# Optimization experiments

Measured on AMD Instinct MI355X. Metric: run time of the kernel, lower is better.

The kernel has to match this reference:

```python
import jax, jax.numpy as jnp
import numpy as np

BN_EPS = 1e-5

def setup_inputs() -> dict:
    key = jax.random.key(0)
    ks = jax.random.split(key, 8)
    B, C, H, W = 32, 256, 64, 64
    Cm, Co = 128, 256  # mid = max(8, 256//2), out = 256
    x = jax.random.normal(ks[0], (B, C, H, W), dtype=jnp.float32)
    w1 = jax.random.normal(ks[1], (Cm, C), dtype=jnp.float32) * 0.05
    b1 = jnp.zeros((Cm,), dtype=jnp.float32)
    bn_gamma = jnp.ones((Cm,), dtype=jnp.float32)
    bn_beta = jnp.zeros((Cm,), dtype=jnp.float32)
    bn_mean = jnp.zeros((Cm,), dtype=jnp.float32)
    bn_var = jnp.ones((Cm,), dtype=jnp.float32)
    w2 = jax.random.normal(ks[2], (Co, Cm), dtype=jnp.float32) * 0.05
    b2 = jnp.zeros((Co,), dtype=jnp.float32)
    w3 = jax.random.normal(ks[3], (Co, Cm), dtype=jnp.float32) * 0.05
    b3 = jnp.zeros((Co,), dtype=jnp.float32)
    return {"x": x, "w1": w1, "b1": b1, "bn_gamma": bn_gamma, "bn_beta": bn_beta,
            "bn_mean": bn_mean, "bn_var": bn_var, "w2": w2, "b2": b2, "w3": w3, "b3": b3}

def _hswish(y):
    return y * jnp.clip(y + 3.0, 0.0, 6.0) / 6.0

def reference(x, w1, b1, bn_gamma, bn_beta, bn_mean, bn_var, w2, b2, w3, b3):
    B, C, H, W = x.shape
    # pool_h: mean over W -> [B,C,H]; pool_w: mean over H -> [B,C,W] (after permute)
    xh = jnp.mean(x, axis=3)  # [B,C,H]
    xw = jnp.mean(x, axis=2)  # [B,C,W]
    y = jnp.concatenate([xh, xw], axis=2)  # [B,C,H+W]
    # 1x1 conv as matmul over channel dim
    y = jnp.einsum('mc,bcl->bml', w1, y) + b1[None, :, None]  # [B,Cm,H+W]
    # BatchNorm (inference, running stats)
    y = (y - bn_mean[None, :, None]) * (bn_gamma[None, :, None] * jax.lax.rsqrt(bn_var + BN_EPS)[None, :, None]) + bn_beta[None, :, None]
    y = _hswish(y)
    ah, aw = y[:, :, :H], y[:, :, H:]  # [B,Cm,H], [B,Cm,W]
    gh = jax.nn.sigmoid(jnp.einsum('om,bmh->boh', w2, ah) + b2[None, :, None])  # [B,Co,H]
    gw = jax.nn.sigmoid(jnp.einsum('om,bmw->bow', w3, aw) + b3[None, :, None])  # [B,Co,W]
    return x * gh[:, :, :, None] * gw[:, :, None, :]
```

## Files before the change

### kernel.cpp

```cpp
#include <hip/hip_runtime.h>

#define NB 32
#define NC 256
#define NL 128
#define NCM 128
#define NCO 256
#define NPLANES (NB * NC)

__global__ __launch_bounds__(256) void k_pool(const float* __restrict__ x,
                                              float* __restrict__ pool) {
    int t = threadIdx.x;
    __shared__ float smem[1024];
    #pragma unroll
    for (int p = 0; p < 4; ++p) {
        int plane = blockIdx.x * 4 + p;
        const float4* px = (const float4*)(x + (size_t)plane * 4096);
        float4 csum = make_float4(0.f, 0.f, 0.f, 0.f);
        #pragma unroll
        for (int i = 0; i < 4; ++i) {
            int f = t + i * 256;
            float4 v = px[f];
            csum.x += v.x; csum.y += v.y; csum.z += v.z; csum.w += v.w;
            float s = v.x + v.y + v.z + v.w;
            s += __shfl_xor(s, 1);
            s += __shfl_xor(s, 2);
            s += __shfl_xor(s, 4);
            s += __shfl_xor(s, 8);
            if ((t & 15) == 0)
                pool[(size_t)plane * NL + (t >> 4) + 16 * i] = s * 0.015625f;
        }
        ((float4*)smem)[t] = csum;
        __syncthreads();
        if (t < 64) {
            float acc = 0.f;
            #pragma unroll
            for (int g = 0; g < 16; ++g)
                acc += smem[((t >> 2) + 16 * g) * 4 + (t & 3)];
            pool[(size_t)plane * NL + 64 + t] = acc * 0.015625f;
        }
        __syncthreads();
    }
}

__global__ __launch_bounds__(256) void k_mlp1(const float* __restrict__ pool,
                                              const float* __restrict__ w1,
                                              const float* __restrict__ b1,
                                              const float* __restrict__ gam,
                                              const float* __restrict__ bet,
                                              const float* __restrict__ mu,
                                              const float* __restrict__ var,
                                              float* __restrict__ a) {
    int b = blockIdx.x, m0 = blockIdx.y * 16;
    int t = threadIdx.x;
    __shared__ float w1t[32][16];
    __shared__ float pt[32][NL];
    const float* poolb = pool + (size_t)b * NC * NL;
    int tm = t & 7;
    int tl = t >> 3;
    float acc[2][4] = {};

    for (int cc = 0; cc < NC; cc += 32) {
        {
            int mi = t & 15, c0 = (t >> 4) * 2;
            float2 wv = *(const float2*)(w1 + (size_t)(m0 + mi) * NC + cc + c0);
            w1t[c0 + 0][mi] = wv.x; w1t[c0 + 1][mi] = wv.y;
        }
        #pragma unroll
        for (int i = 0; i < 4; ++i) {
            int f = t + i * 256;
            int ci = f >> 5, l4 = f & 31;
            *(float4*)&pt[ci][l4 * 4] =
                *(const float4*)(poolb + (size_t)(cc + ci) * NL + l4 * 4);
        }
        __syncthreads();
        #pragma unroll
        for (int cj = 0; cj < 32; ++cj) {
            float2 wv = *(const float2*)&w1t[cj][tm * 2];
            float4 pv = *(const float4*)&pt[cj][tl * 4];
            float pa[4] = {pv.x, pv.y, pv.z, pv.w};
            #pragma unroll
            for (int j = 0; j < 4; ++j) {
                acc[0][j] += wv.x * pa[j];
                acc[1][j] += wv.y * pa[j];
            }
        }
        __syncthreads();
    }
    #pragma unroll
    for (int i = 0; i < 2; ++i) {
        int m = m0 + tm * 2 + i;
        float scale = gam[m] * rsqrtf(var[m] + 1e-5f);
        float base = b1[m] - mu[m];
        float bb = bet[m];
        #pragma unroll
        for (int j = 0; j < 4; ++j) {
            float y = (acc[i][j] + base) * scale + bb;
            float hs = y * fminf(fmaxf(y + 3.f, 0.f), 6.f) * (1.f / 6.f);
            a[(size_t)b * NCM * NL + (size_t)m * NL + tl * 4 + j] = hs;
        }
    }
}

__global__ __launch_bounds__(256) void k_gate(const float* __restrict__ a,
                                              const float* __restrict__ w2,
                                              const float* __restrict__ b2,
                                              const float* __restrict__ w3,
                                              const float* __restrict__ b3,
                                              float* __restrict__ gh,
                                              float* __restrict__ gw) {
    int b = blockIdx.x, side = blockIdx.y, ot = blockIdx.z;
    const float* wsel = side ? w3 : w2;
    const float* bsel = side ? b3 : b2;
    float* gsel = side ? gw : gh;
    int t = threadIdx.x;
    __shared__ float wt[32][32];
    __shared__ float at[32][64];
    int to = t & 15;
    int th = t >> 4;
    float acc[2][4] = {};
    const float* ab = a + (size_t)b * NCM * NL + side * 64;

    for (int kc = 0; kc < NCM; kc += 32) {
        {
            int oi = t & 31, k0 = (t >> 5) * 4;
            float4 wv = *(const float4*)(wsel + (size_t)(ot * 32 + oi) * NCM + kc + k0);
            wt[k0 + 0][oi] = wv.x; wt[k0 + 1][oi] = wv.y;
            wt[k0 + 2][oi] = wv.z; wt[k0 + 3][oi] = wv.w;
        }
        #pragma unroll
        for (int i = 0; i < 2; ++i) {
            int f = t + i * 256;
            int ki = f >> 4, h4 = f & 15;
            *(float4*)&at[ki][h4 * 4] =
                *(const float4*)(ab + (size_t)(kc + ki) * NL + h4 * 4);
        }
        __syncthreads();
        #pragma unroll
        for (int kj = 0; kj < 32; ++kj) {
            float2 wv = *(const float2*)&wt[kj][to * 2];
            float4 av = *(const float4*)&at[kj][th * 4];
            float aa[4] = {av.x, av.y, av.z, av.w};
            #pragma unroll
            for (int j = 0; j < 4; ++j) {
                acc[0][j] += wv.x * aa[j];
                acc[1][j] += wv.y * aa[j];
            }
        }
        __syncthreads();
    }
    #pragma unroll
    for (int i = 0; i < 2; ++i) {
        int o = ot * 32 + to * 2 + i;
        float bias = bsel[o];
        #pragma unroll
        for (int j = 0; j < 4; ++j) {
            float v = acc[i][j] + bias;
            float g = 1.f / (1.f + __expf(-v));
            gsel[((size_t)b * NCO + o) * 64 + th * 4 + j] = g;
        }
    }
}

__global__ __launch_bounds__(256) void k_apply(const float* __restrict__ x,
                                               const float* __restrict__ gh,
                                               const float* __restrict__ gw,
                                               float* __restrict__ out) {
    int t = threadIdx.x;
    #pragma unroll
    for (int p = 0; p < 2; ++p) {
        int plane = blockIdx.x * 2 + p;
        const float4* px = (const float4*)(x + (size_t)plane * 4096);
        float4* po = (float4*)(out + (size_t)plane * 4096);
        const float* ghp = gh + (size_t)plane * 64;
        const float4* gwp = (const float4*)(gw + (size_t)plane * 64);
        #pragma unroll
        for (int i = 0; i < 4; ++i) {
            int f = t + i * 256;
            int row = f >> 4, w4 = f & 15;
            float4 v = px[f];
            float g = ghp[row];
            float4 gv = gwp[w4];
            v.x *= g * gv.x; v.y *= g * gv.y;
            v.z *= g * gv.z; v.w *= g * gv.w;
            po[f] = v;
        }
    }
}

extern "C" void kernel_launch(void* const* d_in, const int* in_sizes, int n_in,
                              void* d_out, int out_size, void* d_ws, size_t ws_size,
                              hipStream_t stream) {
    const float* x   = (const float*)d_in[0];
    const float* w1  = (const float*)d_in[1];
    const float* b1  = (const float*)d_in[2];
    const float* gam = (const float*)d_in[3];
    const float* bet = (const float*)d_in[4];
    const float* mu  = (const float*)d_in[5];
    const float* var = (const float*)d_in[6];
    const float* w2  = (const float*)d_in[7];
    const float* b2  = (const float*)d_in[8];
    const float* w3  = (const float*)d_in[9];
    const float* b3  = (const float*)d_in[10];
    float* ws   = (float*)d_ws;
    float* pool = ws;
    float* a    = ws + 1048576;
    float* gh   = ws + 1572864;
    float* gw   = ws + 2097152;
    float* out  = (float*)d_out;

    k_pool<<<NPLANES / 4, 256, 0, stream>>>(x, pool);
    k_mlp1<<<dim3(NB, 8), 256, 0, stream>>>(pool, w1, b1, gam, bet, mu, var, a);
    k_gate<<<dim3(NB, 2, 8), 256, 0, stream>>>(a, w2, b2, w3, b3, gh, gw);
    k_apply<<<NPLANES / 2, 256, 0, stream>>>(x, gh, gw, out);
}
```

Baseline: 85.87 us.

## Fuse pooling, MLP, gating and apply into one kernel with per-batch barriers

```diff
diff --git a/kernel.cpp b/kernel.cpp
--- a/kernel.cpp
+++ b/kernel.cpp
@@ -6,14 +6,49 @@
 #define NCM 128
 #define NCO 256
 #define NPLANES (NB * NC)
-
-__global__ __launch_bounds__(256) void k_pool(const float* __restrict__ x,
-                                              float* __restrict__ pool) {
-    int t = threadIdx.x;
-    __shared__ float smem[1024];
-    #pragma unroll
-    for (int p = 0; p < 4; ++p) {
-        int plane = blockIdx.x * 4 + p;
+#define SUBS 32
+
+typedef float v4f __attribute__((ext_vector_type(4)));
+
+__device__ __forceinline__ void st_coh(float* p, float v) {
+    __hip_atomic_store(p, v, __ATOMIC_RELAXED, __HIP_MEMORY_SCOPE_AGENT);
+}
+__device__ __forceinline__ float ld_coh(const float* p) {
+    return __hip_atomic_load(p, __ATOMIC_RELAXED, __HIP_MEMORY_SCOPE_AGENT);
+}
+
+__device__ __forceinline__ void batch_barrier(unsigned* cnt) {
+    __syncthreads();
+    if (threadIdx.x == 0) {
+        __hip_atomic_fetch_add(cnt, 1u, __ATOMIC_RELEASE,
+                               __HIP_MEMORY_SCOPE_AGENT);
+        while (__hip_atomic_load(cnt, __ATOMIC_RELAXED,
+                                 __HIP_MEMORY_SCOPE_AGENT) < (unsigned)SUBS)
+            __builtin_amdgcn_s_sleep(2);
+    }
+    __syncthreads();
+}
+
+__global__ __launch_bounds__(256, 4) void k_ca(
+    const float* __restrict__ x,
+    const float* __restrict__ w1, const float* __restrict__ b1,
+    const float* __restrict__ gam, const float* __restrict__ bet,
+    const float* __restrict__ mu, const float* __restrict__ var,
+    const float* __restrict__ w2, const float* __restrict__ b2,
+    const float* __restrict__ w3, const float* __restrict__ b3,
+    float* __restrict__ pool, float* __restrict__ a,
+    float* __restrict__ gh, float* __restrict__ gw,
+    unsigned* __restrict__ bar,
+    float* __restrict__ out)
+{
+    const int blk = blockIdx.x;
+    const int b   = blk >> 5;
+    const int sub = blk & 31;
+    const int t   = threadIdx.x;
+    __shared__ float smem[4608];
+
+    for (int p = 0; p < 8; ++p) {
+        int plane = b * NC + sub * 8 + p;
         const float4* px = (const float4*)(x + (size_t)plane * 4096);
         float4 csum = make_float4(0.f, 0.f, 0.f, 0.f);
         #pragma unroll
@@ -27,7 +62,8 @@
             s += __shfl_xor(s, 4);
             s += __shfl_xor(s, 8);
             if ((t & 15) == 0)
-                pool[(size_t)plane * NL + (t >> 4) + 16 * i] = s * 0.015625f;
+                st_coh(&pool[(size_t)plane * NL + (t >> 4) + 16 * i],
+                       s * 0.015625f);
         }
         ((float4*)smem)[t] = csum;
         __syncthreads();
@@ -36,153 +72,143 @@
             #pragma unroll
             for (int g = 0; g < 16; ++g)
                 acc += smem[((t >> 2) + 16 * g) * 4 + (t & 3)];
-            pool[(size_t)plane * NL + 64 + t] = acc * 0.015625f;
+            st_coh(&pool[(size_t)plane * NL + 64 + t], acc * 0.015625f);
         }
         __syncthreads();
     }
-}
-
-__global__ __launch_bounds__(256) void k_mlp1(const float* __restrict__ pool,
-                                              const float* __restrict__ w1,
-                                              const float* __restrict__ b1,
-                                              const float* __restrict__ gam,
-                                              const float* __restrict__ bet,
-                                              const float* __restrict__ mu,
-                                              const float* __restrict__ var,
-                                              float* __restrict__ a) {
-    int b = blockIdx.x, m0 = blockIdx.y * 16;
-    int t = threadIdx.x;
-    __shared__ float w1t[32][16];
-    __shared__ float pt[32][NL];
-    const float* poolb = pool + (size_t)b * NC * NL;
-    int tm = t & 7;
-    int tl = t >> 3;
-    float acc[2][4] = {};
-
-    for (int cc = 0; cc < NC; cc += 32) {
-        {
-            int mi = t & 15, c0 = (t >> 4) * 2;
-            float2 wv = *(const float2*)(w1 + (size_t)(m0 + mi) * NC + cc + c0);
-            w1t[c0 + 0][mi] = wv.x; w1t[c0 + 1][mi] = wv.y;
-        }
-        #pragma unroll
-        for (int i = 0; i < 4; ++i) {
-            int f = t + i * 256;
-            int ci = f >> 5, l4 = f & 31;
-            *(float4*)&pt[ci][l4 * 4] =
-                *(const float4*)(poolb + (size_t)(cc + ci) * NL + l4 * 4);
+    batch_barrier(&bar[b * 3 + 0]);
+
+    if (sub < 8) {
+        int m0 = sub * 16;
+        float* w1t = smem;
+        float* pt  = smem + 512;
+        const float* poolb = pool + (size_t)b * NC * NL;
+        int tm = t & 7, tl = t >> 3;
+        float acc[2][4] = {};
+        for (int cc = 0; cc < NC; cc += 32) {
+            {
+                int mi = t & 15, c0 = (t >> 4) * 2;
+                float2 wv = *(const float2*)(w1 + (size_t)(m0 + mi) * NC + cc + c0);
+                w1t[(c0 + 0) * 16 + mi] = wv.x;
+                w1t[(c0 + 1) * 16 + mi] = wv.y;
+            }
+            #pragma unroll
+            for (int k = 0; k < 16; ++k) {
+                int idx = t + k * 256;
+                int ci = idx >> 7, l = idx & 127;
+                pt[ci * 128 + l] = ld_coh(poolb + (size_t)(cc + ci) * NL + l);
+            }
+            __syncthreads();
+            #pragma unroll
+            for (int cj = 0; cj < 32; ++cj) {
+                float2 wv = *(const float2*)&w1t[cj * 16 + tm * 2];
+                float4 pv = *(const float4*)&pt[cj * 128 + tl * 4];
+                float pa[4] = {pv.x, pv.y, pv.z, pv.w};
+                #pragma unroll
+                for (int j = 0; j < 4; ++j) {
+                    acc[0][j] += wv.x * pa[j];
+                    acc[1][j] += wv.y * pa[j];
+                }
+            }
+            __syncthreads();
+        }
+        #pragma unroll
+        for (int i = 0; i < 2; ++i) {
+            int m = m0 + tm * 2 + i;
+            float scale = gam[m] * rsqrtf(var[m] + 1e-5f);
+            float base = b1[m] - mu[m];
+            float bb = bet[m];
+            #pragma unroll
+            for (int j = 0; j < 4; ++j) {
+                float y = (acc[i][j] + base) * scale + bb;
+                float hs = y * fminf(fmaxf(y + 3.f, 0.f), 6.f) * (1.f / 6.f);
+                st_coh(&a[(size_t)b * NCM * NL + (size_t)m * NL + tl * 4 + j], hs);
+            }
+        }
+    }
+    batch_barrier(&bar[b * 3 + 1]);
+
+    if (sub < 16) {
+        int side = sub >> 3, ot = sub & 7;
+        const float* wsel = side ? w3 : w2;
+        const float* bsel = side ? b3 : b2;
+        float* gsel = side ? gw : gh;
+        float* wt = smem;
+        float* at = smem + 1024;
+        int to = t & 15, th = t >> 4;
+        float acc[2][4] = {};
+        const float* ab = a + (size_t)b * NCM * NL + side * 64;
+        for (int kc = 0; kc < NCM; kc += 32) {
+            {
+                int oi = t & 31, k0 = (t >> 5) * 4;
+                float4 wv = *(const float4*)(wsel + (size_t)(ot * 32 + oi) * NCM + kc + k0);
+                wt[(k0 + 0) * 32 + oi] = wv.x; wt[(k0 + 1) * 32 + oi] = wv.y;
+                wt[(k0 + 2) * 32 + oi] = wv.z; wt[(k0 + 3) * 32 + oi] = wv.w;
+            }
+            #pragma unroll
+            for (int k = 0; k < 8; ++k) {
+                int idx = t + k * 256;
+                int ki = idx >> 6, h = idx & 63;
+                at[ki * 64 + h] = ld_coh(ab + (size_t)(kc + ki) * NL + h);
+            }
+            __syncthreads();
+            #pragma unroll
+            for (int kj = 0; kj < 32; ++kj) {
+                float2 wv = *(const float2*)&wt[kj * 32 + to * 2];
+                float4 av = *(const float4*)&at[kj * 64 + th * 4];
+                float aa[4] = {av.x, av.y, av.z, av.w};
+                #pragma unroll
+                for (int j = 0; j < 4; ++j) {
+                    acc[0][j] += wv.x * aa[j];
+                    acc[1][j] += wv.y * aa[j];
+                }
+            }
+            __syncthreads();
+        }
+        #pragma unroll
+        for (int i = 0; i < 2; ++i) {
+            int o = ot * 32 + to * 2 + i;
+            float bias = bsel[o];
+            #pragma unroll
+            for (int j = 0; j < 4; ++j) {
+                float v = acc[i][j] + bias;
+                float g = 1.f / (1.f + __expf(-v));
+                st_coh(&gsel[((size_t)b * NCO + o) * 64 + th * 4 + j], g);
+            }
+        }
+    }
+    batch_barrier(&bar[b * 3 + 2]);
+
+    {
+        float* gsm = smem;
+        int c0 = sub * 8;
+        #pragma unroll
+        for (int k = 0; k < 4; ++k) {
+            int idx = t + k * 256;
+            int p = idx >> 7, r = idx & 127;
+            size_t plane = (size_t)b * NC + c0 + p;
+            float v = (r < 64) ? ld_coh(&gh[plane * 64 + r])
+                               : ld_coh(&gw[plane * 64 + (r - 64)]);
+            gsm[p * 128 + r] = v;
         }
         __syncthreads();
-        #pragma unroll
-        for (int cj = 0; cj < 32; ++cj) {
-            float2 wv = *(const float2*)&w1t[cj][tm * 2];
-            float4 pv = *(const float4*)&pt[cj][tl * 4];
-            float pa[4] = {pv.x, pv.y, pv.z, pv.w};
-            #pragma unroll
-            for (int j = 0; j < 4; ++j) {
-                acc[0][j] += wv.x * pa[j];
-                acc[1][j] += wv.y * pa[j];
-            }
-        }
-        __syncthreads();
-    }
-    #pragma unroll
-    for (int i = 0; i < 2; ++i) {
-        int m = m0 + tm * 2 + i;
-        float scale = gam[m] * rsqrtf(var[m] + 1e-5f);
-        float base = b1[m] - mu[m];
-        float bb = bet[m];
-        #pragma unroll
-        for (int j = 0; j < 4; ++j) {
-            float y = (acc[i][j] + base) * scale + bb;
-            float hs = y * fminf(fmaxf(y + 3.f, 0.f), 6.f) * (1.f / 6.f);
-            a[(size_t)b * NCM * NL + (size_t)m * NL + tl * 4 + j] = hs;
-        }
-    }
-}
-
-__global__ __launch_bounds__(256) void k_gate(const float* __restrict__ a,
-                                              const float* __restrict__ w2,
-                                              const float* __restrict__ b2,
-                                              const float* __restrict__ w3,
-                                              const float* __restrict__ b3,
-                                              float* __restrict__ gh,
-                                              float* __restrict__ gw) {
-    int b = blockIdx.x, side = blockIdx.y, ot = blockIdx.z;
-    const float* wsel = side ? w3 : w2;
-    const float* bsel = side ? b3 : b2;
-    float* gsel = side ? gw : gh;
-    int t = threadIdx.x;
-    __shared__ float wt[32][32];
-    __shared__ float at[32][64];
-    int to = t & 15;
-    int th = t >> 4;
-    float acc[2][4] = {};
-    const float* ab = a + (size_t)b * NCM * NL + side * 64;
-
-    for (int kc = 0; kc < NCM; kc += 32) {
-        {
-            int oi = t & 31, k0 = (t >> 5) * 4;
-            float4 wv = *(const float4*)(wsel + (size_t)(ot * 32 + oi) * NCM + kc + k0);
-            wt[k0 + 0][oi] = wv.x; wt[k0 + 1][oi] = wv.y;
-            wt[k0 + 2][oi] = wv.z; wt[k0 + 3][oi] = wv.w;
-        }
-        #pragma unroll
-        for (int i = 0; i < 2; ++i) {
-            int f = t + i * 256;
-            int ki = f >> 4, h4 = f & 15;
-            *(float4*)&at[ki][h4 * 4] =
-                *(const float4*)(ab + (size_t)(kc + ki) * NL + h4 * 4);
-        }
-        __syncthreads();
-        #pragma unroll
-        for (int kj = 0; kj < 32; ++kj) {
-            float2 wv = *(const float2*)&wt[kj][to * 2];
-            float4 av = *(const float4*)&at[kj][th * 4];
-            float aa[4] = {av.x, av.y, av.z, av.w};
-            #pragma unroll
-            for (int j = 0; j < 4; ++j) {
-                acc[0][j] += wv.x * aa[j];
-                acc[1][j] += wv.y * aa[j];
-            }
-        }
-        __syncthreads();
-    }
-    #pragma unroll
-    for (int i = 0; i < 2; ++i) {
-        int o = ot * 32 + to * 2 + i;
-        float bias = bsel[o];
-        #pragma unroll
-        for (int j = 0; j < 4; ++j) {
-            float v = acc[i][j] + bias;
-            float g = 1.f / (1.f + __expf(-v));
-            gsel[((size_t)b * NCO + o) * 64 + th * 4 + j] = g;
-        }
-    }
-}
-
-__global__ __launch_bounds__(256) void k_apply(const float* __restrict__ x,
-                                               const float* __restrict__ gh,
-                                               const float* __restrict__ gw,
-                                               float* __restrict__ out) {
-    int t = threadIdx.x;
-    #pragma unroll
-    for (int p = 0; p < 2; ++p) {
-        int plane = blockIdx.x * 2 + p;
-        const float4* px = (const float4*)(x + (size_t)plane * 4096);
-        float4* po = (float4*)(out + (size_t)plane * 4096);
-        const float* ghp = gh + (size_t)plane * 64;
-        const float4* gwp = (const float4*)(gw + (size_t)plane * 64);
-        #pragma unroll
-        for (int i = 0; i < 4; ++i) {
-            int f = t + i * 256;
-            int row = f >> 4, w4 = f & 15;
-            float4 v = px[f];
-            float g = ghp[row];
-            float4 gv = gwp[w4];
-            v.x *= g * gv.x; v.y *= g * gv.y;
-            v.z *= g * gv.z; v.w *= g * gv.w;
-            po[f] = v;
+        for (int p = 0; p < 8; ++p) {
+            size_t plane = (size_t)b * NC + c0 + p;
+            const float4* px = (const float4*)(x + plane * 4096);
+            float4* po = (float4*)(out + plane * 4096);
+            const float* ghp = &gsm[p * 128];
+            const float4* gwp = (const float4*)&gsm[p * 128 + 64];
+            #pragma unroll
+            for (int i = 0; i < 4; ++i) {
+                int f = t + i * 256;
+                int row = f >> 4, w4 = f & 15;
+                float4 v = px[f];
+                float g = ghp[row];
+                float4 gv = gwp[w4];
+                v.x *= g * gv.x; v.y *= g * gv.y;
+                v.z *= g * gv.z; v.w *= g * gv.w;
+                po[f] = v;
+            }
         }
     }
 }
@@ -206,10 +232,11 @@
     float* a    = ws + 1048576;
     float* gh   = ws + 1572864;
     float* gw   = ws + 2097152;
+    unsigned* bar = (unsigned*)(ws + 2621440);
     float* out  = (float*)d_out;
 
-    k_pool<<<NPLANES / 4, 256, 0, stream>>>(x, pool);
-    k_mlp1<<<dim3(NB, 8), 256, 0, stream>>>(pool, w1, b1, gam, bet, mu, var, a);
-    k_gate<<<dim3(NB, 2, 8), 256, 0, stream>>>(a, w2, b2, w3, b3, gh, gw);
-    k_apply<<<NPLANES / 2, 256, 0, stream>>>(x, gh, gw, out);
-}
+    hipMemsetAsync(bar, 0, NB * 3 * sizeof(unsigned), stream);
+    k_ca<<<NB * SUBS, 256, 0, stream>>>(x, w1, b1, gam, bet, mu, var,
+                                        w2, b2, w3, b3,
+                                        pool, a, gh, gw, bar, out);
+}
```

After: 287.3 us. 235% more time.

## Fuse channel MLP and gate kernels, per-wave pooling without block sync

Applied to the files above, without the earlier changes.

```diff
diff --git a/kernel.cpp b/kernel.cpp
--- a/kernel.cpp
+++ b/kernel.cpp
@@ -7,157 +7,150 @@
 #define NCO 256
 #define NPLANES (NB * NC)
 
+typedef float v4f __attribute__((ext_vector_type(4)));
+
 __global__ __launch_bounds__(256) void k_pool(const float* __restrict__ x,
                                               float* __restrict__ pool) {
-    int t = threadIdx.x;
-    __shared__ float smem[1024];
-    #pragma unroll
-    for (int p = 0; p < 4; ++p) {
-        int plane = blockIdx.x * 4 + p;
-        const float4* px = (const float4*)(x + (size_t)plane * 4096);
-        float4 csum = make_float4(0.f, 0.f, 0.f, 0.f);
-        #pragma unroll
-        for (int i = 0; i < 4; ++i) {
-            int f = t + i * 256;
-            float4 v = px[f];
-            csum.x += v.x; csum.y += v.y; csum.z += v.z; csum.w += v.w;
-            float s = v.x + v.y + v.z + v.w;
-            s += __shfl_xor(s, 1);
-            s += __shfl_xor(s, 2);
-            s += __shfl_xor(s, 4);
-            s += __shfl_xor(s, 8);
-            if ((t & 15) == 0)
-                pool[(size_t)plane * NL + (t >> 4) + 16 * i] = s * 0.015625f;
-        }
-        ((float4*)smem)[t] = csum;
-        __syncthreads();
-        if (t < 64) {
-            float acc = 0.f;
-            #pragma unroll
-            for (int g = 0; g < 16; ++g)
-                acc += smem[((t >> 2) + 16 * g) * 4 + (t & 3)];
-            pool[(size_t)plane * NL + 64 + t] = acc * 0.015625f;
-        }
-        __syncthreads();
-    }
-}
-
-__global__ __launch_bounds__(256) void k_mlp1(const float* __restrict__ pool,
-                                              const float* __restrict__ w1,
-                                              const float* __restrict__ b1,
-                                              const float* __restrict__ gam,
-                                              const float* __restrict__ bet,
-                                              const float* __restrict__ mu,
-                                              const float* __restrict__ var,
-                                              float* __restrict__ a) {
-    int b = blockIdx.x, m0 = blockIdx.y * 16;
-    int t = threadIdx.x;
-    __shared__ float w1t[32][16];
-    __shared__ float pt[32][NL];
-    const float* poolb = pool + (size_t)b * NC * NL;
-    int tm = t & 7;
-    int tl = t >> 3;
-    float acc[2][4] = {};
-
-    for (int cc = 0; cc < NC; cc += 32) {
-        {
-            int mi = t & 15, c0 = (t >> 4) * 2;
-            float2 wv = *(const float2*)(w1 + (size_t)(m0 + mi) * NC + cc + c0);
-            w1t[c0 + 0][mi] = wv.x; w1t[c0 + 1][mi] = wv.y;
-        }
-        #pragma unroll
-        for (int i = 0; i < 4; ++i) {
-            int f = t + i * 256;
-            int ci = f >> 5, l4 = f & 31;
-            *(float4*)&pt[ci][l4 * 4] =
-                *(const float4*)(poolb + (size_t)(cc + ci) * NL + l4 * 4);
-        }
-        __syncthreads();
-        #pragma unroll
-        for (int cj = 0; cj < 32; ++cj) {
-            float2 wv = *(const float2*)&w1t[cj][tm * 2];
-            float4 pv = *(const float4*)&pt[cj][tl * 4];
-            float pa[4] = {pv.x, pv.y, pv.z, pv.w};
-            #pragma unroll
-            for (int j = 0; j < 4; ++j) {
-                acc[0][j] += wv.x * pa[j];
-                acc[1][j] += wv.y * pa[j];
-            }
-        }
-        __syncthreads();
-    }
-    #pragma unroll
-    for (int i = 0; i < 2; ++i) {
-        int m = m0 + tm * 2 + i;
-        float scale = gam[m] * rsqrtf(var[m] + 1e-5f);
-        float base = b1[m] - mu[m];
-        float bb = bet[m];
-        #pragma unroll
-        for (int j = 0; j < 4; ++j) {
-            float y = (acc[i][j] + base) * scale + bb;
-            float hs = y * fminf(fmaxf(y + 3.f, 0.f), 6.f) * (1.f / 6.f);
-            a[(size_t)b * NCM * NL + (size_t)m * NL + tl * 4 + j] = hs;
-        }
-    }
-}
-
-__global__ __launch_bounds__(256) void k_gate(const float* __restrict__ a,
-                                              const float* __restrict__ w2,
-                                              const float* __restrict__ b2,
-                                              const float* __restrict__ w3,
-                                              const float* __restrict__ b3,
-                                              float* __restrict__ gh,
-                                              float* __restrict__ gw) {
-    int b = blockIdx.x, side = blockIdx.y, ot = blockIdx.z;
+    int wid  = threadIdx.x >> 6;
+    int lane = threadIdx.x & 63;
+    int plane = blockIdx.x * 4 + wid;
+    const float4* px = (const float4*)(x + (size_t)plane * 4096);
+    float* pp = pool + (size_t)plane * NL;
+
+    float4 csum = make_float4(0.f, 0.f, 0.f, 0.f);
+    #pragma unroll
+    for (int i = 0; i < 16; ++i) {
+        int f = lane + i * 64;
+        float4 v = px[f];
+        csum.x += v.x; csum.y += v.y; csum.z += v.z; csum.w += v.w;
+        float s = v.x + v.y + v.z + v.w;
+        s += __shfl_xor(s, 1);
+        s += __shfl_xor(s, 2);
+        s += __shfl_xor(s, 4);
+        s += __shfl_xor(s, 8);
+        if ((lane & 15) == 0)
+            pp[(lane >> 4) + 4 * i] = s * 0.015625f;
+    }
+    csum.x += __shfl_xor(csum.x, 16); csum.y += __shfl_xor(csum.y, 16);
+    csum.z += __shfl_xor(csum.z, 16); csum.w += __shfl_xor(csum.w, 16);
+    csum.x += __shfl_xor(csum.x, 32); csum.y += __shfl_xor(csum.y, 32);
+    csum.z += __shfl_xor(csum.z, 32); csum.w += __shfl_xor(csum.w, 32);
+    if (lane < 16) {
+        float4 r = make_float4(csum.x * 0.015625f, csum.y * 0.015625f,
+                               csum.z * 0.015625f, csum.w * 0.015625f);
+        *(float4*)&pp[64 + lane * 4] = r;
+    }
+}
+
+__global__ __launch_bounds__(256) void k_mid(const float* __restrict__ pool,
+                                             const float* __restrict__ w1,
+                                             const float* __restrict__ b1,
+                                             const float* __restrict__ gam,
+                                             const float* __restrict__ bet,
+                                             const float* __restrict__ mu,
+                                             const float* __restrict__ var,
+                                             const float* __restrict__ w2,
+                                             const float* __restrict__ b2,
+                                             const float* __restrict__ w3,
+                                             const float* __restrict__ b3,
+                                             float* __restrict__ gh,
+                                             float* __restrict__ gw) {
+    const int b = blockIdx.x, side = blockIdx.y;
+    const int t = threadIdx.x;
     const float* wsel = side ? w3 : w2;
     const float* bsel = side ? b3 : b2;
     float* gsel = side ? gw : gh;
-    int t = threadIdx.x;
-    __shared__ float wt[32][32];
-    __shared__ float at[32][64];
-    int to = t & 15;
-    int th = t >> 4;
-    float acc[2][4] = {};
-    const float* ab = a + (size_t)b * NCM * NL + side * 64;
-
-    for (int kc = 0; kc < NCM; kc += 32) {
-        {
-            int oi = t & 31, k0 = (t >> 5) * 4;
-            float4 wv = *(const float4*)(wsel + (size_t)(ot * 32 + oi) * NCM + kc + k0);
-            wt[k0 + 0][oi] = wv.x; wt[k0 + 1][oi] = wv.y;
-            wt[k0 + 2][oi] = wv.z; wt[k0 + 3][oi] = wv.w;
-        }
-        #pragma unroll
-        for (int i = 0; i < 2; ++i) {
-            int f = t + i * 256;
-            int ki = f >> 4, h4 = f & 15;
-            *(float4*)&at[ki][h4 * 4] =
-                *(const float4*)(ab + (size_t)(kc + ki) * NL + h4 * 4);
+    const float* poolb = pool + (size_t)b * NC * NL + side * 64;
+
+    __shared__ float sm[8704];
+    float* pt   = sm;
+    float* a_sm = sm;
+
+    int tm = t & 31, tl = t >> 5;
+    float acc[4][8] = {};
+    for (int cc = 0; cc < NC; cc += 64) {
+        #pragma unroll
+        for (int k = 0; k < 4; ++k) {
+            int fidx = t + k * 256;
+            int ci = fidx >> 4, l4 = fidx & 15;
+            float4 v = *(const float4*)(poolb + (size_t)(cc + ci) * NL + l4 * 4);
+            *(float4*)&pt[ci * 68 + l4 * 4] = v;
         }
         __syncthreads();
-        #pragma unroll
-        for (int kj = 0; kj < 32; ++kj) {
-            float2 wv = *(const float2*)&wt[kj][to * 2];
-            float4 av = *(const float4*)&at[kj][th * 4];
-            float aa[4] = {av.x, av.y, av.z, av.w};
+        #pragma unroll 4
+        for (int cj4 = 0; cj4 < 16; ++cj4) {
+            v4f wv[4];
             #pragma unroll
-            for (int j = 0; j < 4; ++j) {
-                acc[0][j] += wv.x * aa[j];
-                acc[1][j] += wv.y * aa[j];
+            for (int i = 0; i < 4; ++i)
+                wv[i] = *(const v4f*)(w1 + (size_t)(tm * 4 + i) * NC + cc + cj4 * 4);
+            #pragma unroll
+            for (int cjj = 0; cjj < 4; ++cjj) {
+                int cj = cj4 * 4 + cjj;
+                float4 p0 = *(const float4*)&pt[cj * 68 + tl * 8];
+                float4 p1 = *(const float4*)&pt[cj * 68 + tl * 8 + 4];
+                float pa[8] = {p0.x, p0.y, p0.z, p0.w, p1.x, p1.y, p1.z, p1.w};
+                #pragma unroll
+                for (int i = 0; i < 4; ++i) {
+                    float w = wv[i][cjj];
+                    #pragma unroll
+                    for (int j = 0; j < 8; ++j)
+                        acc[i][j] += w * pa[j];
+                }
             }
         }
         __syncthreads();
     }
     #pragma unroll
-    for (int i = 0; i < 2; ++i) {
-        int o = ot * 32 + to * 2 + i;
+    for (int i = 0; i < 4; ++i) {
+        int m = tm * 4 + i;
+        float scale = gam[m] * rsqrtf(var[m] + 1e-5f);
+        float base  = b1[m] - mu[m];
+        float bb    = bet[m];
+        float r[8];
+        #pragma unroll
+        for (int j = 0; j < 8; ++j) {
+            float y = (acc[i][j] + base) * scale + bb;
+            r[j] = y * fminf(fmaxf(y + 3.f, 0.f), 6.f) * (1.f / 6.f);
+        }
+        *(float4*)&a_sm[m * 68 + tl * 8]     = make_float4(r[0], r[1], r[2], r[3]);
+        *(float4*)&a_sm[m * 68 + tl * 8 + 4] = make_float4(r[4], r[5], r[6], r[7]);
+    }
+    __syncthreads();
+
+    int to = t & 31, tlb = t >> 5;
+    float acc2[8][8] = {};
+    #pragma unroll 2
+    for (int mj4 = 0; mj4 < 32; ++mj4) {
+        v4f wv[8];
+        #pragma unroll
+        for (int i = 0; i < 8; ++i)
+            wv[i] = *(const v4f*)(wsel + (size_t)(to * 8 + i) * NCM + mj4 * 4);
+        #pragma unroll
+        for (int mjj = 0; mjj < 4; ++mjj) {
+            int mj = mj4 * 4 + mjj;
+            float4 a0 = *(const float4*)&a_sm[mj * 68 + tlb * 8];
+            float4 a1 = *(const float4*)&a_sm[mj * 68 + tlb * 8 + 4];
+            float aa[8] = {a0.x, a0.y, a0.z, a0.w, a1.x, a1.y, a1.z, a1.w};
+            #pragma unroll
+            for (int i = 0; i < 8; ++i) {
+                float w = wv[i][mjj];
+                #pragma unroll
+                for (int j = 0; j < 8; ++j)
+                    acc2[i][j] += w * aa[j];
+            }
+        }
+    }
+    #pragma unroll
+    for (int i = 0; i < 8; ++i) {
+        int o = to * 8 + i;
         float bias = bsel[o];
-        #pragma unroll
-        for (int j = 0; j < 4; ++j) {
-            float v = acc[i][j] + bias;
-            float g = 1.f / (1.f + __expf(-v));
-            gsel[((size_t)b * NCO + o) * 64 + th * 4 + j] = g;
-        }
+        float g[8];
+        #pragma unroll
+        for (int j = 0; j < 8; ++j)
+            g[j] = 1.f / (1.f + __expf(-(acc2[i][j] + bias)));
+        float* gp = gsel + ((size_t)b * NCO + o) * 64 + tlb * 8;
+        *(float4*)&gp[0] = make_float4(g[0], g[1], g[2], g[3]);
+        *(float4*)&gp[4] = make_float4(g[4], g[5], g[6], g[7]);
     }
 }
 
@@ -203,13 +196,12 @@
     const float* b3  = (const float*)d_in[10];
     float* ws   = (float*)d_ws;
     float* pool = ws;
-    float* a    = ws + 1048576;
-    float* gh   = ws + 1572864;
-    float* gw   = ws + 2097152;
+    float* gh   = ws + 1048576;
+    float* gw   = ws + 1572864;
     float* out  = (float*)d_out;
 
     k_pool<<<NPLANES / 4, 256, 0, stream>>>(x, pool);
-    k_mlp1<<<dim3(NB, 8), 256, 0, stream>>>(pool, w1, b1, gam, bet, mu, var, a);
-    k_gate<<<dim3(NB, 2, 8), 256, 0, stream>>>(a, w2, b2, w3, b3, gh, gw);
+    k_mid<<<dim3(NB, 2), 256, 0, stream>>>(pool, w1, b1, gam, bet, mu, var,
+                                           w2, b2, w3, b3, gh, gw);
     k_apply<<<NPLANES / 2, 256, 0, stream>>>(x, gh, gw, out);
 }
```

Measured after the change: 131.9 us. +53.6%, slower.

## Restructure MLP kernels to stage weights in LDS and stream activations directly

Applied to the files above, without the earlier changes.

```diff
diff --git a/kernel.cpp b/kernel.cpp
--- a/kernel.cpp
+++ b/kernel.cpp
@@ -50,55 +50,42 @@
                                               const float* __restrict__ mu,
                                               const float* __restrict__ var,
                                               float* __restrict__ a) {
-    int b = blockIdx.x, m0 = blockIdx.y * 16;
+    int b = blockIdx.x, m0 = blockIdx.y * 8;
     int t = threadIdx.x;
-    __shared__ float w1t[32][16];
-    __shared__ float pt[32][NL];
-    const float* poolb = pool + (size_t)b * NC * NL;
-    int tm = t & 7;
-    int tl = t >> 3;
-    float acc[2][4] = {};
+    __shared__ float w1s[8 * 256];
+    #pragma unroll
+    for (int k = 0; k < 2; ++k) {
+        int idx = t + k * 256;
+        int r = idx >> 6, c4 = idx & 63;
+        *(float4*)&w1s[r * 256 + c4 * 4] =
+            *(const float4*)(w1 + (size_t)(m0 + r) * NC + c4 * 4);
+    }
+    __syncthreads();
 
-    for (int cc = 0; cc < NC; cc += 32) {
-        {
-            int mi = t & 15, c0 = (t >> 4) * 2;
-            float2 wv = *(const float2*)(w1 + (size_t)(m0 + mi) * NC + cc + c0);
-            w1t[c0 + 0][mi] = wv.x; w1t[c0 + 1][mi] = wv.y;
-        }
-        #pragma unroll
-        for (int i = 0; i < 4; ++i) {
-            int f = t + i * 256;
-            int ci = f >> 5, l4 = f & 31;
-            *(float4*)&pt[ci][l4 * 4] =
-                *(const float4*)(poolb + (size_t)(cc + ci) * NL + l4 * 4);
-        }
-        __syncthreads();
-        #pragma unroll
-        for (int cj = 0; cj < 32; ++cj) {
-            float2 wv = *(const float2*)&w1t[cj][tm * 2];
-            float4 pv = *(const float4*)&pt[cj][tl * 4];
-            float pa[4] = {pv.x, pv.y, pv.z, pv.w};
-            #pragma unroll
-            for (int j = 0; j < 4; ++j) {
-                acc[0][j] += wv.x * pa[j];
-                acc[1][j] += wv.y * pa[j];
-            }
-        }
-        __syncthreads();
+    int l4 = t & 31;
+    int mh = t >> 5;
+    const float* pb = pool + (size_t)b * NC * NL + l4 * 4;
+    const float* wr = &w1s[mh * 256];
+    float acc[4] = {};
+    #pragma unroll 8
+    for (int c = 0; c < NC; ++c) {
+        float4 pv = *(const float4*)(pb + (size_t)c * NL);
+        float w = wr[c];
+        acc[0] += w * pv.x; acc[1] += w * pv.y;
+        acc[2] += w * pv.z; acc[3] += w * pv.w;
     }
+    int m = m0 + mh;
+    float scale = gam[m] * rsqrtf(var[m] + 1e-5f);
+    float base  = b1[m] - mu[m];
+    float bb    = bet[m];
+    float r[4];
     #pragma unroll
-    for (int i = 0; i < 2; ++i) {
-        int m = m0 + tm * 2 + i;
-        float scale = gam[m] * rsqrtf(var[m] + 1e-5f);
-        float base = b1[m] - mu[m];
-        float bb = bet[m];
-        #pragma unroll
-        for (int j = 0; j < 4; ++j) {
-            float y = (acc[i][j] + base) * scale + bb;
-            float hs = y * fminf(fmaxf(y + 3.f, 0.f), 6.f) * (1.f / 6.f);
-            a[(size_t)b * NCM * NL + (size_t)m * NL + tl * 4 + j] = hs;
-        }
+    for (int j = 0; j < 4; ++j) {
+        float y = (acc[j] + base) * scale + bb;
+        r[j] = y * fminf(fmaxf(y + 3.f, 0.f), 6.f) * (1.f / 6.f);
     }
+    *(float4*)(a + (size_t)b * NCM * NL + (size_t)m * NL + l4 * 4) =
+        make_float4(r[0], r[1], r[2], r[3]);
 }
 
 __global__ __launch_bounds__(256) void k_gate(const float* __restrict__ a,
@@ -108,56 +95,46 @@
                                               const float* __restrict__ b3,
                                               float* __restrict__ gh,
                                               float* __restrict__ gw) {
-    int b = blockIdx.x, side = blockIdx.y, ot = blockIdx.z;
+    int b = blockIdx.x, side = blockIdx.y, o0 = blockIdx.z * 32;
     const float* wsel = side ? w3 : w2;
     const float* bsel = side ? b3 : b2;
     float* gsel = side ? gw : gh;
     int t = threadIdx.x;
-    __shared__ float wt[32][32];
-    __shared__ float at[32][64];
-    int to = t & 15;
-    int th = t >> 4;
+    __shared__ float wsm[32 * 128];
+    #pragma unroll
+    for (int k = 0; k < 4; ++k) {
+        int idx = t + k * 256;
+        int r = idx >> 5, m4 = idx & 31;
+        *(float4*)&wsm[r * 128 + m4 * 4] =
+            *(const float4*)(wsel + (size_t)(o0 + r) * NCM + m4 * 4);
+    }
+    __syncthreads();
+
+    int l4 = t & 15;
+    int oh = t >> 4;
+    const float* ab = a + (size_t)b * NCM * NL + side * 64 + l4 * 4;
+    const float* w0 = &wsm[(oh * 2 + 0) * 128];
+    const float* w1r = &wsm[(oh * 2 + 1) * 128];
     float acc[2][4] = {};
-    const float* ab = a + (size_t)b * NCM * NL + side * 64;
-
-    for (int kc = 0; kc < NCM; kc += 32) {
-        {
-            int oi = t & 31, k0 = (t >> 5) * 4;
-            float4 wv = *(const float4*)(wsel + (size_t)(ot * 32 + oi) * NCM + kc + k0);
-            wt[k0 + 0][oi] = wv.x; wt[k0 + 1][oi] = wv.y;
-            wt[k0 + 2][oi] = wv.z; wt[k0 + 3][oi] = wv.w;
-        }
-        #pragma unroll
-        for (int i = 0; i < 2; ++i) {
-            int f = t + i * 256;
-            int ki = f >> 4, h4 = f & 15;
-            *(float4*)&at[ki][h4 * 4] =
-                *(const float4*)(ab + (size_t)(kc + ki) * NL + h4 * 4);
-        }
-        __syncthreads();
-        #pragma unroll
-        for (int kj = 0; kj < 32; ++kj) {
-            float2 wv = *(const float2*)&wt[kj][to * 2];
-            float4 av = *(const float4*)&at[kj][th * 4];
-            float aa[4] = {av.x, av.y, av.z, av.w};
-            #pragma unroll
-            for (int j = 0; j < 4; ++j) {
-                acc[0][j] += wv.x * aa[j];
-                acc[1][j] += wv.y * aa[j];
-            }
-        }
-        __syncthreads();
+    #pragma unroll 8
+    for (int m = 0; m < NCM; ++m) {
+        float4 av = *(const float4*)(ab + (size_t)m * NL);
+        float wa = w0[m], wb = w1r[m];
+        acc[0][0] += wa * av.x; acc[0][1] += wa * av.y;
+        acc[0][2] += wa * av.z; acc[0][3] += wa * av.w;
+        acc[1][0] += wb * av.x; acc[1][1] += wb * av.y;
+        acc[1][2] += wb * av.z; acc[1][3] += wb * av.w;
     }
     #pragma unroll
     for (int i = 0; i < 2; ++i) {
-        int o = ot * 32 + to * 2 + i;
+        int o = o0 + oh * 2 + i;
         float bias = bsel[o];
+        float g[4];
         #pragma unroll
-        for (int j = 0; j < 4; ++j) {
-            float v = acc[i][j] + bias;
-            float g = 1.f / (1.f + __expf(-v));
-            gsel[((size_t)b * NCO + o) * 64 + th * 4 + j] = g;
-        }
+        for (int j = 0; j < 4; ++j)
+            g[j] = 1.f / (1.f + __expf(-(acc[i][j] + bias)));
+        *(float4*)(gsel + ((size_t)b * NCO + o) * 64 + l4 * 4) =
+            make_float4(g[0], g[1], g[2], g[3]);
     }
 }
 
@@ -209,7 +186,7 @@
     float* out  = (float*)d_out;
 
     k_pool<<<NPLANES / 4, 256, 0, stream>>>(x, pool);
-    k_mlp1<<<dim3(NB, 8), 256, 0, stream>>>(pool, w1, b1, gam, bet, mu, var, a);
+    k_mlp1<<<dim3(NB, 16), 256, 0, stream>>>(pool, w1, b1, gam, bet, mu, var, a);
     k_gate<<<dim3(NB, 2, 8), 256, 0, stream>>>(a, w2, b2, w3, b3, gh, gw);
     k_apply<<<NPLANES / 2, 256, 0, stream>>>(x, gh, gw, out);
 }
```

New measurement: 92.43 us. +7.6%, slower.
